# Kernel tuning notes

Hardware: AMD Instinct MI355X
Metric: run time of the kernel (lower is better)

The kernel has to match this reference:

```python
import jax, jax.numpy as jnp
import numpy as np

B, S, H = 4, 2048, 1024  # batch, seq, hidden


def setup_inputs() -> dict:
    key = jax.random.key(0)
    kq, kk, kv = jax.random.split(key, 3)
    return {
        "Q": jax.random.normal(kq, (B, S, H), dtype=jnp.float32),
        "K": jax.random.normal(kk, (B, S, H), dtype=jnp.float32),
        "V": jax.random.normal(kv, (B, S, H), dtype=jnp.float32),
    }


def reference(Q, K, V):
    # Phase of rfft along hidden dim -> [B, S, F], F = H//2 + 1
    q_fft = jnp.fft.rfft(Q, axis=-1)
    k_fft = jnp.fft.rfft(K, axis=-1)
    q_phase = jnp.arctan2(q_fft.imag, q_fft.real)
    k_phase = jnp.arctan2(k_fft.imag, k_fft.real)
    n_freqs = q_phase.shape[-1]
    # mean_f cos(qp_i - kp_j) = (cos(qp) @ cos(kp)^T + sin(qp) @ sin(kp)^T) / F
    # Avoids materializing the [B,S,S,F] phase_diff tensor; math is identical.
    align = (
        jnp.einsum("bif,bjf->bij", jnp.cos(q_phase), jnp.cos(k_phase))
        + jnp.einsum("bif,bjf->bij", jnp.sin(q_phase), jnp.sin(k_phase))
    ) / n_freqs
    scores = align + 1.0
    weights = jax.nn.softmax(scores, axis=-1)  # [B, S, S]
    output = jnp.einsum("bij,bjh->bih", weights, V)  # [B, S, H]
    return output, weights
```

## Files before the change

kernel.cpp:

```cpp
#include <hip/hip_runtime.h>
#include <hip/hip_bf16.h>
#include <math.h>

#define Bb 4
#define Ss 2048
#define Hh 1024
#define Ff 513
#define FEAT 1026
#define KP2 1056

typedef __attribute__((ext_vector_type(8))) short bf16x8;
typedef __attribute__((ext_vector_type(4))) float f32x4;

typedef const __attribute__((address_space(1))) void GVoid;
typedef __attribute__((address_space(3))) void LVoid;

#define PADI(i) ((i) + ((i) >> 4))

__device__ __forceinline__ float2 cmul(float2 a, float2 b) {
  return make_float2(a.x * b.x - a.y * b.y, a.x * b.y + a.y * b.x);
}

__global__ __launch_bounds__(256) void fft_phase_kernel(
    const float* __restrict__ Q, const float* __restrict__ Kin,
    __hip_bfloat16* __restrict__ FQ, __hip_bfloat16* __restrict__ FK) {
  const int row = blockIdx.x;
  const float* qs = Q   + (size_t)row * Hh;
  const float* ks = Kin + (size_t)row * Hh;
  __hip_bfloat16* fq = FQ + (size_t)row * KP2;
  __hip_bfloat16* fk = FK + (size_t)row * KP2;

  __shared__ float2 data[PADI(1023) + 1];
  __shared__ float2 tw[1024];
  const int tid = threadIdx.x;

#pragma unroll
  for (int e = 0; e < 4; ++e) {
    const int m = tid + e * 256;
    float s, c;
    sincosf(-6.283185307179586f * (float)m * (1.0f / 1024.0f), &s, &c);
    tw[m] = make_float2(c, s);
  }
#pragma unroll
  for (int e = 0; e < 4; ++e) {
    const int n = tid + e * 256;
    const int r4 = ((n & 3) << 8) | (((n >> 2) & 3) << 6) | (((n >> 4) & 3) << 4)
                 | (((n >> 6) & 3) << 2) | ((n >> 8) & 3);
    data[PADI(r4)] = make_float2(qs[n], ks[n]);
  }
  __syncthreads();

  int quarter = 1, step = 256;
  for (int s = 0; s < 5; ++s) {
    const int j = tid & (quarter - 1);
    const int pos = 4 * tid - 3 * j;
    const float2 x0 = data[PADI(pos)];
    const float2 x1 = data[PADI(pos + quarter)];
    const float2 x2 = data[PADI(pos + 2 * quarter)];
    const float2 x3 = data[PADI(pos + 3 * quarter)];
    const int e1 = j * step;
    const float2 a1 = cmul(x1, tw[e1]);
    const float2 a2 = cmul(x2, tw[2 * e1]);
    const float2 a3 = cmul(x3, tw[3 * e1]);
    const float2 t0 = make_float2(x0.x + a2.x, x0.y + a2.y);
    const float2 t1 = make_float2(x0.x - a2.x, x0.y - a2.y);
    const float2 t2 = make_float2(a1.x + a3.x, a1.y + a3.y);
    const float2 t3 = make_float2(a1.x - a3.x, a1.y - a3.y);
    data[PADI(pos)]               = make_float2(t0.x + t2.x, t0.y + t2.y);
    data[PADI(pos + quarter)]     = make_float2(t1.x + t3.y, t1.y - t3.x);
    data[PADI(pos + 2 * quarter)] = make_float2(t0.x - t2.x, t0.y - t2.y);
    data[PADI(pos + 3 * quarter)] = make_float2(t1.x - t3.y, t1.y + t3.x);
    __syncthreads();
    quarter <<= 2; step >>= 2;
  }

  for (int f = tid; f <= 512; f += 256) {
    const float2 z1 = data[PADI(f)];
    const float2 z2 = data[PADI((1024 - f) & 1023)];
    const float qr = z1.x + z2.x, qi = z1.y - z2.y;
    const float kr = z1.y + z2.y, ki = z2.x - z1.x;
    float qc, qsn, kc, ksn;
    const float qm2 = qr * qr + qi * qi;
    if (qm2 > 1e-30f) { const float iv = rsqrtf(qm2); qc = qr * iv; qsn = qi * iv; }
    else              { qc = 1.0f; qsn = 0.0f; }
    const float km2 = kr * kr + ki * ki;
    if (km2 > 1e-30f) { const float iv = rsqrtf(km2); kc = kr * iv; ksn = ki * iv; }
    else              { kc = 1.0f; ksn = 0.0f; }
    fq[f] = __float2bfloat16(qc); fq[Ff + f] = __float2bfloat16(qsn);
    fk[f] = __float2bfloat16(kc); fk[Ff + f] = __float2bfloat16(ksn);
  }
  for (int p = FEAT + tid; p < KP2; p += 256) {
    fq[p] = __float2bfloat16(0.0f);
    fk[p] = __float2bfloat16(0.0f);
  }
}

__global__ __launch_bounds__(256) void vt_kernel(
    const float* __restrict__ V, __hip_bfloat16* __restrict__ Vt) {
  const int b = blockIdx.z;
  const int h0 = blockIdx.x * 32;
  const int s0 = blockIdx.y * 32;
  __shared__ float t[32][33];
  const int tid = threadIdx.x;
  const int c = tid & 31;
  const int r8 = tid >> 5;
  const float* Vb = V + (size_t)b * Ss * Hh;
#pragma unroll
  for (int e = 0; e < 4; ++e) {
    const int r = r8 + e * 8;
    t[r][c] = Vb[(size_t)(s0 + r) * Hh + h0 + c];
  }
  __syncthreads();
  __hip_bfloat16* O = Vt + (size_t)b * Hh * Ss;
#pragma unroll
  for (int e = 0; e < 4; ++e) {
    const int hh = r8 + e * 8;
    O[(size_t)(h0 + hh) * Ss + s0 + c] = __float2bfloat16(t[c][hh]);
  }
}

template<int K, int LDA, int LDB, int LDC, int EPI>
__global__ __launch_bounds__(256) void gemm_bt(
    const __hip_bfloat16* __restrict__ Ag, const __hip_bfloat16* __restrict__ Bg,
    float* __restrict__ Cg, size_t strA, size_t strB, size_t strC) {
  const int b = blockIdx.z;
  const int i0 = blockIdx.y * 128;
  const int j0 = blockIdx.x * 128;
  const char* Ab = (const char*)(Ag + (size_t)b * strA);
  const char* Bp = (const char*)(Bg + (size_t)b * strB);
  float* C = Cg + (size_t)b * strC;

  __shared__ short As[4096];
  __shared__ short Bs[4096];

  const int tid = threadIdx.x;
  const int lane = tid & 63;
  const int w = tid >> 6;
  const int wm = w >> 1, wn = w & 1;
  const int lrow = lane & 15;
  const int lchunk = lane >> 4;

  f32x4 acc[4][4];
#pragma unroll
  for (int m = 0; m < 4; ++m)
#pragma unroll
    for (int n = 0; n < 4; ++n)
      acc[m][n] = (f32x4){0.0f, 0.0f, 0.0f, 0.0f};

  const size_t aoff0 = (size_t)(i0 + (w    ) * 16 + lrow) * (LDA * 2) + lchunk * 16;
  const size_t aoff1 = (size_t)(i0 + (w + 4) * 16 + lrow) * (LDA * 2) + lchunk * 16;
  const size_t boff0 = (size_t)(j0 + (w    ) * 16 + lrow) * (LDB * 2) + lchunk * 16;
  const size_t boff1 = (size_t)(j0 + (w + 4) * 16 + lrow) * (LDB * 2) + lchunk * 16;

  for (int k0 = 0; k0 < K; k0 += 32) {
    __syncthreads();
    const size_t kb = (size_t)k0 * 2;
    __builtin_amdgcn_global_load_lds((GVoid*)(Ab + aoff0 + kb), (LVoid*)&As[(w    ) * 512], 16, 0, 0);
    __builtin_amdgcn_global_load_lds((GVoid*)(Ab + aoff1 + kb), (LVoid*)&As[(w + 4) * 512], 16, 0, 0);
    __builtin_amdgcn_global_load_lds((GVoid*)(Bp + boff0 + kb), (LVoid*)&Bs[(w    ) * 512], 16, 0, 0);
    __builtin_amdgcn_global_load_lds((GVoid*)(Bp + boff1 + kb), (LVoid*)&Bs[(w + 4) * 512], 16, 0, 0);
    __syncthreads();

    bf16x8 af[4], bfr[4];
#pragma unroll
    for (int m = 0; m < 4; ++m)
      af[m] = *(const bf16x8*)&As[(wm * 4 + m) * 512 + lchunk * 128 + lrow * 8];
#pragma unroll
    for (int n = 0; n < 4; ++n)
      bfr[n] = *(const bf16x8*)&Bs[(wn * 4 + n) * 512 + lchunk * 128 + lrow * 8];
#pragma unroll
    for (int m = 0; m < 4; ++m)
#pragma unroll
      for (int n = 0; n < 4; ++n)
        acc[m][n] = __builtin_amdgcn_mfma_f32_16x16x32_bf16(af[m], bfr[n], acc[m][n], 0, 0, 0);
  }

  const int r4 = (lane >> 4) * 4;
  const int cc = lane & 15;
#pragma unroll
  for (int m = 0; m < 4; ++m) {
    const int ib = i0 + wm * 64 + m * 16 + r4;
#pragma unroll
    for (int n = 0; n < 4; ++n) {
      const int j = j0 + wn * 64 + n * 16 + cc;
#pragma unroll
      for (int r = 0; r < 4; ++r) {
        float v = acc[m][n][r];
        if (EPI == 0) v = v * (1.0f / 513.0f);
        C[(size_t)(ib + r) * LDC + j] = v;
      }
    }
  }
}

__global__ __launch_bounds__(256) void softmax_kernel(
    float* __restrict__ W, __hip_bfloat16* __restrict__ Wb) {
  const size_t row = blockIdx.x;
  float* p = W + row * (size_t)Ss;
  __hip_bfloat16* pb = Wb + row * (size_t)Ss;
  const int tid = threadIdx.x;
  __shared__ float red[4];

  float v[8];
  float m = -3.0e38f;
#pragma unroll
  for (int e = 0; e < 8; ++e) { v[e] = p[tid + e * 256]; m = fmaxf(m, v[e]); }
#pragma unroll
  for (int off = 32; off > 0; off >>= 1) m = fmaxf(m, __shfl_down(m, off, 64));
  if ((tid & 63) == 0) red[tid >> 6] = m;
  __syncthreads();
  m = fmaxf(fmaxf(red[0], red[1]), fmaxf(red[2], red[3]));

  float sum = 0.0f;
#pragma unroll
  for (int e = 0; e < 8; ++e) { v[e] = expf(v[e] - m); sum += v[e]; }
#pragma unroll
  for (int off = 32; off > 0; off >>= 1) sum += __shfl_down(sum, off, 64);
  __syncthreads();
  if ((tid & 63) == 0) red[tid >> 6] = sum;
  __syncthreads();
  sum = red[0] + red[1] + red[2] + red[3];

  const float rs = 1.0f / sum;
#pragma unroll
  for (int e = 0; e < 8; ++e) {
    const float o = v[e] * rs;
    p[tid + e * 256] = o;
    pb[tid + e * 256] = __float2bfloat16(o);
  }
}

extern "C" void kernel_launch(void* const* d_in, const int* in_sizes, int n_in,
                              void* d_out, int out_size, void* d_ws, size_t ws_size,
                              hipStream_t stream) {
  const float* Q = (const float*)d_in[0];
  const float* K = (const float*)d_in[1];
  const float* V = (const float*)d_in[2];

  float* out     = (float*)d_out;
  float* weights = out + (size_t)Bb * Ss * Hh;

  __hip_bfloat16* FQb = (__hip_bfloat16*)d_ws;
  __hip_bfloat16* FKb = FQb + (size_t)Bb * Ss * KP2;
  __hip_bfloat16* Vtb = FKb + (size_t)Bb * Ss * KP2;
  __hip_bfloat16* Wb  = (__hip_bfloat16*)d_ws;

  hipLaunchKernelGGL(fft_phase_kernel, dim3(Bb * Ss), dim3(256), 0, stream,
                     Q, K, FQb, FKb);
  hipLaunchKernelGGL(vt_kernel, dim3(Hh / 32, Ss / 32, Bb), dim3(256), 0, stream,
                     V, Vtb);
  hipLaunchKernelGGL((gemm_bt<KP2, KP2, KP2, Ss, 0>), dim3(16, 16, Bb), dim3(256), 0, stream,
                     FQb, FKb, weights,
                     (size_t)Ss * KP2, (size_t)Ss * KP2, (size_t)Ss * Ss);
  hipLaunchKernelGGL(softmax_kernel, dim3(Bb * Ss), dim3(256), 0, stream,
                     weights, Wb);
  hipLaunchKernelGGL((gemm_bt<Ss, Ss, Ss, Hh, 1>), dim3(8, 16, Bb), dim3(256), 0, stream,
                     Wb, Vtb, out,
                     (size_t)Ss * Ss, (size_t)Hh * Ss, (size_t)Ss * Hh);
}
```

Before: 204.1 us.

## Double-buffer GEMM LDS tiles and vectorize softmax loads and stores

The bf16 GEMM now uses two LDS buffers per operand and issues the global-to-LDS loads for the next K slice before computing on the current one. This removes one barrier per iteration and lets load latency overlap with the MFMA work. The softmax kernel changes to float4 loads and stores, packs its eight bf16 outputs into one 16-byte store, and uses __expf and xor shuffles. The costs are doubled LDS per block and a cheaper, less precise exponential.

```diff
diff --git a/kernel.cpp b/kernel.cpp
--- a/kernel.cpp
+++ b/kernel.cpp
@@ -19,6 +19,11 @@
 
 __device__ __forceinline__ float2 cmul(float2 a, float2 b) {
   return make_float2(a.x * b.x - a.y * b.y, a.x * b.y + a.y * b.x);
+}
+
+__device__ __forceinline__ unsigned short bf16bits(float x) {
+  __hip_bfloat16 h = __float2bfloat16(x);
+  return *reinterpret_cast<unsigned short*>(&h);
 }
 
 __global__ __launch_bounds__(256) void fft_phase_kernel(
@@ -130,8 +135,8 @@
   const char* Bp = (const char*)(Bg + (size_t)b * strB);
   float* C = Cg + (size_t)b * strC;
 
-  __shared__ short As[4096];
-  __shared__ short Bs[4096];
+  __shared__ short As[2][4096];
+  __shared__ short Bs[2][4096];
 
   const int tid = threadIdx.x;
   const int lane = tid & 63;
@@ -152,28 +157,39 @@
   const size_t boff0 = (size_t)(j0 + (w    ) * 16 + lrow) * (LDB * 2) + lchunk * 16;
   const size_t boff1 = (size_t)(j0 + (w + 4) * 16 + lrow) * (LDB * 2) + lchunk * 16;
 
+#define STAGE(buf, k0)                                                                              \
+  do {                                                                                              \
+    const size_t kb = (size_t)(k0) * 2;                                                             \
+    __builtin_amdgcn_global_load_lds((GVoid*)(Ab + aoff0 + kb), (LVoid*)&As[buf][(w    ) * 512], 16, 0, 0); \
+    __builtin_amdgcn_global_load_lds((GVoid*)(Ab + aoff1 + kb), (LVoid*)&As[buf][(w + 4) * 512], 16, 0, 0); \
+    __builtin_amdgcn_global_load_lds((GVoid*)(Bp + boff0 + kb), (LVoid*)&Bs[buf][(w    ) * 512], 16, 0, 0); \
+    __builtin_amdgcn_global_load_lds((GVoid*)(Bp + boff1 + kb), (LVoid*)&Bs[buf][(w + 4) * 512], 16, 0, 0); \
+  } while (0)
+
+  STAGE(0, 0);
+  __syncthreads();
+  int cur = 0;
+
   for (int k0 = 0; k0 < K; k0 += 32) {
-    __syncthreads();
-    const size_t kb = (size_t)k0 * 2;
-    __builtin_amdgcn_global_load_lds((GVoid*)(Ab + aoff0 + kb), (LVoid*)&As[(w    ) * 512], 16, 0, 0);
-    __builtin_amdgcn_global_load_lds((GVoid*)(Ab + aoff1 + kb), (LVoid*)&As[(w + 4) * 512], 16, 0, 0);
-    __builtin_amdgcn_global_load_lds((GVoid*)(Bp + boff0 + kb), (LVoid*)&Bs[(w    ) * 512], 16, 0, 0);
-    __builtin_amdgcn_global_load_lds((GVoid*)(Bp + boff1 + kb), (LVoid*)&Bs[(w + 4) * 512], 16, 0, 0);
-    __syncthreads();
+    if (k0 + 32 < K) STAGE(cur ^ 1, k0 + 32);
 
     bf16x8 af[4], bfr[4];
 #pragma unroll
     for (int m = 0; m < 4; ++m)
-      af[m] = *(const bf16x8*)&As[(wm * 4 + m) * 512 + lchunk * 128 + lrow * 8];
+      af[m] = *(const bf16x8*)&As[cur][(wm * 4 + m) * 512 + lchunk * 128 + lrow * 8];
 #pragma unroll
     for (int n = 0; n < 4; ++n)
-      bfr[n] = *(const bf16x8*)&Bs[(wn * 4 + n) * 512 + lchunk * 128 + lrow * 8];
+      bfr[n] = *(const bf16x8*)&Bs[cur][(wn * 4 + n) * 512 + lchunk * 128 + lrow * 8];
 #pragma unroll
     for (int m = 0; m < 4; ++m)
 #pragma unroll
       for (int n = 0; n < 4; ++n)
         acc[m][n] = __builtin_amdgcn_mfma_f32_16x16x32_bf16(af[m], bfr[n], acc[m][n], 0, 0, 0);
-  }
+
+    __syncthreads();
+    cur ^= 1;
+  }
+#undef STAGE
 
   const int r4 = (lane >> 4) * 4;
   const int cc = lane & 15;
@@ -201,21 +217,25 @@
   const int tid = threadIdx.x;
   __shared__ float red[4];
 
-  float v[8];
-  float m = -3.0e38f;
-#pragma unroll
-  for (int e = 0; e < 8; ++e) { v[e] = p[tid + e * 256]; m = fmaxf(m, v[e]); }
-#pragma unroll
-  for (int off = 32; off > 0; off >>= 1) m = fmaxf(m, __shfl_down(m, off, 64));
+  const float4* p4 = (const float4*)p;
+  const float4 a = p4[2 * tid];
+  const float4 bq = p4[2 * tid + 1];
+  float v[8] = {a.x, a.y, a.z, a.w, bq.x, bq.y, bq.z, bq.w};
+
+  float m = v[0];
+#pragma unroll
+  for (int e = 1; e < 8; ++e) m = fmaxf(m, v[e]);
+#pragma unroll
+  for (int off = 32; off > 0; off >>= 1) m = fmaxf(m, __shfl_xor(m, off, 64));
   if ((tid & 63) == 0) red[tid >> 6] = m;
   __syncthreads();
   m = fmaxf(fmaxf(red[0], red[1]), fmaxf(red[2], red[3]));
 
   float sum = 0.0f;
 #pragma unroll
-  for (int e = 0; e < 8; ++e) { v[e] = expf(v[e] - m); sum += v[e]; }
-#pragma unroll
-  for (int off = 32; off > 0; off >>= 1) sum += __shfl_down(sum, off, 64);
+  for (int e = 0; e < 8; ++e) { v[e] = __expf(v[e] - m); sum += v[e]; }
+#pragma unroll
+  for (int off = 32; off > 0; off >>= 1) sum += __shfl_xor(sum, off, 64);
   __syncthreads();
   if ((tid & 63) == 0) red[tid >> 6] = sum;
   __syncthreads();
@@ -223,11 +243,16 @@
 
   const float rs = 1.0f / sum;
 #pragma unroll
-  for (int e = 0; e < 8; ++e) {
-    const float o = v[e] * rs;
-    p[tid + e * 256] = o;
-    pb[tid + e * 256] = __float2bfloat16(o);
-  }
+  for (int e = 0; e < 8; ++e) v[e] *= rs;
+
+  float4* o4 = (float4*)p;
+  o4[2 * tid]     = make_float4(v[0], v[1], v[2], v[3]);
+  o4[2 * tid + 1] = make_float4(v[4], v[5], v[6], v[7]);
+
+  bf16x8 ob;
+#pragma unroll
+  for (int e = 0; e < 8; ++e) ob[e] = (short)bf16bits(v[e]);
+  *(bf16x8*)&pb[8 * tid] = ob;
 }
 
 extern "C" void kernel_launch(void* const* d_in, const int* in_sizes, int n_in,
```

Result: slower. 210.2 us (+3.0%).
